# Performance work log

Hardware: AMD Instinct MI355X
Metric: run time of the kernel (lower is better)

## Reference

```python
import jax, jax.numpy as jnp
import numpy as np


def setup_inputs() -> dict:
    key = jax.random.key(0)
    x = jax.random.normal(key, (4096, 8192), dtype=jnp.float32)
    return {"x": x, "window_size": 64}


def reference(x, window_size):
    # Rolling population std over axis=1, window w, output [B, T-w+1].
    # Single-pass prefix-sum formulation: E[x^2] - E[x]^2 (same math as
    # sqrt(mean((x-mean)^2)) in the original layer, O(T) instead of O(T*w)).
    w = window_size
    B = x.shape[0]
    zero = jnp.zeros((B, 1), dtype=x.dtype)
    c1 = jnp.concatenate([zero, jnp.cumsum(x, axis=1)], axis=1)        # [B, T+1]
    c2 = jnp.concatenate([zero, jnp.cumsum(x * x, axis=1)], axis=1)    # [B, T+1]
    s1 = c1[:, w:] - c1[:, :-w]   # window sums        [B, T-w+1]
    s2 = c2[:, w:] - c2[:, :-w]   # window sum-squares [B, T-w+1]
    mean = s1 / w
    var = jnp.maximum(s2 / w - mean * mean, 0.0)  # clamp fp roundoff
    return jnp.sqrt(var)
```

## Files before the change

### kernel.cpp

```cpp
#include <hip/hip_runtime.h>
#include <math.h>


constexpr int T     = 8192;
constexpr int W     = 64;
constexpr int OUTW  = T - W + 1;
constexpr int NT    = 256;
constexpr int CHUNK = 32;

__global__ __launch_bounds__(NT, 5)
void MovingStandardDeviation_23682449670506_kernel(const float* __restrict__ x,
                                                   float* __restrict__ out) {
    __shared__ float lds[T];
    const int t = threadIdx.x;
    const size_t b = blockIdx.x;
    const float* rowp = x + b * (size_t)T;

    {
        const int srow = (t >> 3) & 7;
        const int sb = (4 * t) ^ (srow << 2);
        #pragma unroll
        for (int i = 0; i < 8; ++i) {
            const float4 v = *reinterpret_cast<const float4*>(rowp + 4 * t + 1024 * i);
            *reinterpret_cast<float4*>(lds + sb + 1024 * i) = v;
        }
    }
    __syncthreads();

    const int j0  = t * CHUNK;
    const int bk0 = j0;
    const int bk1 = min(j0 + 32, T - 32);
    const int bk2 = min(j0 + 64, T - 32);

    float4 q[8];
    {
        const int r0 = (bk0 >> 5) & 7;
        const int A0 = bk0 + (r0 << 2);
        #pragma unroll
        for (int c = 0; c < 8; ++c)
            q[c] = *reinterpret_cast<const float4*>(lds + (A0 ^ (c << 2)));
    }

    float s1, s2;
    {
        float a0 = 0.f, a1 = 0.f, a2 = 0.f, a3 = 0.f;
        float b0 = 0.f, b1 = 0.f, b2 = 0.f, b3 = 0.f;
        #pragma unroll
        for (int c = 0; c < 8; ++c) {
            a0 += q[c].x; b0 = fmaf(q[c].x, q[c].x, b0);
            a1 += q[c].y; b1 = fmaf(q[c].y, q[c].y, b1);
            a2 += q[c].z; b2 = fmaf(q[c].z, q[c].z, b2);
            a3 += q[c].w; b3 = fmaf(q[c].w, q[c].w, b3);
        }
        const int r1 = (bk1 >> 5) & 7;
        const int A1 = bk1 + (r1 << 2);
        #pragma unroll
        for (int c = 0; c < 8; ++c) {
            const float4 v = *reinterpret_cast<const float4*>(lds + (A1 ^ (c << 2)));
            a0 += v.x; b0 = fmaf(v.x, v.x, b0);
            a1 += v.y; b1 = fmaf(v.y, v.y, b1);
            a2 += v.z; b2 = fmaf(v.z, v.z, b2);
            a3 += v.w; b3 = fmaf(v.w, v.w, b3);
        }
        s1 = (a0 + a1) + (a2 + a3);
        s2 = (b0 + b1) + (b2 + b3);
    }

    float res[CHUNK];
    const float invw = 1.0f / (float)W;
    {
        const float mean = s1 * invw;
        res[0] = sqrtf(fmaxf(fmaf(-mean, mean, s2 * invw), 0.f));
    }
    {
        const int r2 = (bk2 >> 5) & 7;
        const int A2 = bk2 + (r2 << 2);
        #pragma unroll
        for (int c = 0; c < 8; ++c) {
            const float4 vin = *reinterpret_cast<const float4*>(lds + (A2 ^ (c << 2)));
            #pragma unroll
            for (int e = 0; e < 4; ++e) {
                const int jj = 4 * c + e + 1;
                if (jj < CHUNK) {
                    const float xin  = (e == 0) ? vin.x : (e == 1) ? vin.y
                                     : (e == 2) ? vin.z : vin.w;
                    const int p = jj - 1;
                    const float4 qq = q[p >> 2];
                    const float xout = ((p & 3) == 0) ? qq.x : ((p & 3) == 1) ? qq.y
                                     : ((p & 3) == 2) ? qq.z : qq.w;
                    const float d = xin - xout;
                    s1 += d;
                    s2 = fmaf(d, xin + xout, s2);
                    const float mean = s1 * invw;
                    res[jj] = sqrtf(fmaxf(fmaf(-mean, mean, s2 * invw), 0.f));
                }
            }
        }
    }
    __syncthreads();

    {
        const int A = 32 * t + ((t & 7) << 2);
        #pragma unroll
        for (int c = 0; c < 8; ++c) {
            const float4 v = make_float4(res[4 * c], res[4 * c + 1],
                                         res[4 * c + 2], res[4 * c + 3]);
            *reinterpret_cast<float4*>(lds + (A ^ (c << 2))) = v;
        }
    }
    __syncthreads();

    {
        const int srow = (t >> 5) & 7;
        const int base = t ^ (srow << 2);
        float* orow = out + b * (size_t)OUTW;
        #pragma unroll
        for (int i = 0; i < 32; ++i) {
            const int j = t + 256 * i;
            const float f = lds[base + 256 * i];
            if (j < OUTW) __builtin_nontemporal_store(f, orow + j);
        }
    }
}

extern "C" void kernel_launch(void* const* d_in, const int* in_sizes, int n_in,
                              void* d_out, int out_size, void* d_ws, size_t ws_size,
                              hipStream_t stream) {
    const float* x = (const float*)d_in[0];
    float* out = (float*)d_out;
    const int B = in_sizes[0] / T;
    MovingStandardDeviation_23682449670506_kernel<<<B, NT, 0, stream>>>(x, out);
}
```

Baseline: 52.09 us.

## Split each row across two blocks with halo staging and smaller per-thread chunks

Each row is now processed by two blocks, each covering half the outputs and staging 4096 plus a 64-element halo in LDS. Each thread handles 16 outputs instead of 32, which cuts register use, and the occupancy hint rises from 5 to 8. The grid doubles, trading some redundant halo loads for more parallelism and more in-flight memory traffic. Nontemporal output stores are replaced with normal stores.

```diff
diff --git a/kernel.cpp b/kernel.cpp
--- a/kernel.cpp
+++ b/kernel.cpp
@@ -6,39 +6,45 @@
 constexpr int W     = 64;
 constexpr int OUTW  = T - W + 1;
 constexpr int NT    = 256;
-constexpr int CHUNK = 32;
+constexpr int HALF  = 4096;
+constexpr int STAGE = 4160;
 
-__global__ __launch_bounds__(NT, 5)
+__global__ __launch_bounds__(NT, 8)
 void MovingStandardDeviation_23682449670506_kernel(const float* __restrict__ x,
                                                    float* __restrict__ out) {
-    __shared__ float lds[T];
+    __shared__ float lds[STAGE];
     const int t = threadIdx.x;
-    const size_t b = blockIdx.x;
+    const int h = blockIdx.x & 1;
+    const size_t b = blockIdx.x >> 1;
+    const int base = h * HALF;
     const float* rowp = x + b * (size_t)T;
 
     {
-        const int srow = (t >> 3) & 7;
-        const int sb = (4 * t) ^ (srow << 2);
+        const int rx = ((t >> 3) & 7) << 2;
         #pragma unroll
-        for (int i = 0; i < 8; ++i) {
-            const float4 v = *reinterpret_cast<const float4*>(rowp + 4 * t + 1024 * i);
-            *reinterpret_cast<float4*>(lds + sb + 1024 * i) = v;
+        for (int l = 0; l < 4; ++l) {
+            const int e = 4 * t + 1024 * l;
+            const int src = min(base + e, T - 4);
+            const float4 v = *reinterpret_cast<const float4*>(rowp + src);
+            *reinterpret_cast<float4*>(lds + (e ^ rx)) = v;
+        }
+        if (t < 16) {
+            const int e = 4096 + 4 * t;
+            const int src = min(base + e, T - 4);
+            const float4 v = *reinterpret_cast<const float4*>(rowp + src);
+            *reinterpret_cast<float4*>(lds + (e ^ rx)) = v;
         }
     }
     __syncthreads();
 
-    const int j0  = t * CHUNK;
-    const int bk0 = j0;
-    const int bk1 = min(j0 + 32, T - 32);
-    const int bk2 = min(j0 + 64, T - 32);
+    const int j0l = 16 * t;
 
-    float4 q[8];
+    float4 q[4];
     {
-        const int r0 = (bk0 >> 5) & 7;
-        const int A0 = bk0 + (r0 << 2);
+        const int rxg = ((j0l >> 5) & 7) << 2;
         #pragma unroll
-        for (int c = 0; c < 8; ++c)
-            q[c] = *reinterpret_cast<const float4*>(lds + (A0 ^ (c << 2)));
+        for (int c = 0; c < 4; ++c)
+            q[c] = *reinterpret_cast<const float4*>(lds + ((j0l + 4 * c) ^ rxg));
     }
 
     float s1, s2;
@@ -46,48 +52,50 @@
         float a0 = 0.f, a1 = 0.f, a2 = 0.f, a3 = 0.f;
         float b0 = 0.f, b1 = 0.f, b2 = 0.f, b3 = 0.f;
         #pragma unroll
-        for (int c = 0; c < 8; ++c) {
+        for (int c = 0; c < 4; ++c) {
             a0 += q[c].x; b0 = fmaf(q[c].x, q[c].x, b0);
             a1 += q[c].y; b1 = fmaf(q[c].y, q[c].y, b1);
             a2 += q[c].z; b2 = fmaf(q[c].z, q[c].z, b2);
             a3 += q[c].w; b3 = fmaf(q[c].w, q[c].w, b3);
         }
-        const int r1 = (bk1 >> 5) & 7;
-        const int A1 = bk1 + (r1 << 2);
         #pragma unroll
-        for (int c = 0; c < 8; ++c) {
-            const float4 v = *reinterpret_cast<const float4*>(lds + (A1 ^ (c << 2)));
-            a0 += v.x; b0 = fmaf(v.x, v.x, b0);
-            a1 += v.y; b1 = fmaf(v.y, v.y, b1);
-            a2 += v.z; b2 = fmaf(v.z, v.z, b2);
-            a3 += v.w; b3 = fmaf(v.w, v.w, b3);
+        for (int gi = 1; gi < 4; ++gi) {
+            const int g = j0l + 16 * gi;
+            const int rxg = ((g >> 5) & 7) << 2;
+            #pragma unroll
+            for (int c = 0; c < 4; ++c) {
+                const float4 v = *reinterpret_cast<const float4*>(lds + ((g + 4 * c) ^ rxg));
+                a0 += v.x; b0 = fmaf(v.x, v.x, b0);
+                a1 += v.y; b1 = fmaf(v.y, v.y, b1);
+                a2 += v.z; b2 = fmaf(v.z, v.z, b2);
+                a3 += v.w; b3 = fmaf(v.w, v.w, b3);
+            }
         }
         s1 = (a0 + a1) + (a2 + a3);
         s2 = (b0 + b1) + (b2 + b3);
     }
 
-    float res[CHUNK];
+    float res[16];
     const float invw = 1.0f / (float)W;
     {
         const float mean = s1 * invw;
         res[0] = sqrtf(fmaxf(fmaf(-mean, mean, s2 * invw), 0.f));
     }
     {
-        const int r2 = (bk2 >> 5) & 7;
-        const int A2 = bk2 + (r2 << 2);
+        const int g4 = j0l + 64;
+        const int rx4 = ((g4 >> 5) & 7) << 2;
         #pragma unroll
-        for (int c = 0; c < 8; ++c) {
-            const float4 vin = *reinterpret_cast<const float4*>(lds + (A2 ^ (c << 2)));
+        for (int c = 0; c < 4; ++c) {
+            const float4 vin = *reinterpret_cast<const float4*>(lds + ((g4 + 4 * c) ^ rx4));
             #pragma unroll
             for (int e = 0; e < 4; ++e) {
                 const int jj = 4 * c + e + 1;
-                if (jj < CHUNK) {
+                if (jj < 16) {
                     const float xin  = (e == 0) ? vin.x : (e == 1) ? vin.y
                                      : (e == 2) ? vin.z : vin.w;
-                    const int p = jj - 1;
-                    const float4 qq = q[p >> 2];
-                    const float xout = ((p & 3) == 0) ? qq.x : ((p & 3) == 1) ? qq.y
-                                     : ((p & 3) == 2) ? qq.z : qq.w;
+                    const float4 qq = q[c];
+                    const float xout = (e == 0) ? qq.x : (e == 1) ? qq.y
+                                     : (e == 2) ? qq.z : qq.w;
                     const float d = xin - xout;
                     s1 += d;
                     s2 = fmaf(d, xin + xout, s2);
@@ -100,25 +108,25 @@
     __syncthreads();
 
     {
-        const int A = 32 * t + ((t & 7) << 2);
+        const int rxw = ((t >> 1) & 7) << 2;
         #pragma unroll
-        for (int c = 0; c < 8; ++c) {
+        for (int c = 0; c < 4; ++c) {
             const float4 v = make_float4(res[4 * c], res[4 * c + 1],
                                          res[4 * c + 2], res[4 * c + 3]);
-            *reinterpret_cast<float4*>(lds + (A ^ (c << 2))) = v;
+            *reinterpret_cast<float4*>(lds + ((16 * t + 4 * c) ^ rxw)) = v;
         }
     }
     __syncthreads();
 
     {
-        const int srow = (t >> 5) & 7;
-        const int base = t ^ (srow << 2);
-        float* orow = out + b * (size_t)OUTW;
+        const int sbase = t ^ (((t >> 5) & 7) << 2);
+        float* orow = out + b * (size_t)OUTW + base;
+        const int lim = OUTW - base;
         #pragma unroll
-        for (int i = 0; i < 32; ++i) {
+        for (int i = 0; i < 16; ++i) {
             const int j = t + 256 * i;
-            const float f = lds[base + 256 * i];
-            if (j < OUTW) __builtin_nontemporal_store(f, orow + j);
+            const float f = lds[sbase + 256 * i];
+            if (j < lim) orow[j] = f;
         }
     }
 }
@@ -129,5 +137,5 @@
     const float* x = (const float*)d_in[0];
     float* out = (float*)d_out;
     const int B = in_sizes[0] / T;
-    MovingStandardDeviation_23682449670506_kernel<<<B, NT, 0, stream>>>(x, out);
+    MovingStandardDeviation_23682449670506_kernel<<<2 * B, NT, 0, stream>>>(x, out);
 }
```

Measured after the change: 47.65 us. 8.5% less time.
